# Kernel optimization log

Measured on AMD Instinct MI355X. Metric: run time of the kernel, lower is better.

## Reference

```python
import jax, jax.numpy as jnp
import numpy as np

SCALES = (3, 5, 7)

def _avg_pool3d_same(x, k):
    # stride-1 avg_pool3d with padding k//2, count_include_pad=True (torch default).
    # For odd k <= dim this preserves the spatial size, so the subsequent
    # F.interpolate to the input size is an exact identity.
    p = k // 2
    s = jax.lax.reduce_window(
        x, 0.0, jax.lax.add,
        window_dimensions=(1, 1, k, k, k),
        window_strides=(1, 1, 1, 1, 1),
        padding=[(0, 0), (0, 0), (p, p), (p, p), (p, p)])
    return s * (1.0 / float(k ** 3))

def setup_inputs() -> dict:
    key = jax.random.key(0)
    k1, k2 = jax.random.split(key)
    B, C, D, H, W = 2, 48, 64, 64, 64
    x = jax.random.normal(k1, (B, C, D, H, W), dtype=jnp.float32)
    fuse_w = jax.random.normal(k2, (1, len(SCALES) * C), dtype=jnp.float32) * 0.05
    fuse_b = jnp.zeros((1,), dtype=jnp.float32)
    return {"x": x, "fuse_w": fuse_w, "fuse_b": fuse_b}

def reference(x, fuse_w, fuse_b):
    # Multi-scale stride-1 average pooling (sizes preserved -> interp is identity)
    pooled = [_avg_pool3d_same(x, k) for k in SCALES]   # each (B, C, D, H, W)
    cat = jnp.concatenate(pooled, axis=1)               # (B, 3C, D, H, W)
    # 1x1x1 conv to a single channel, then sigmoid
    out = jnp.einsum('bcdhw,oc->bodhw', cat, fuse_w) + fuse_b[None, :, None, None, None]
    return jax.nn.sigmoid(out)                          # (B, 1, D, H, W)
```

## Files before the change

### kernel.cpp

```cpp
#include <hip/hip_runtime.h>
#include <math.h>

#define CH       48
#define DIM      64
#define SPATIAL  (DIM * DIM * DIM)
#define NB       2
#define VOL      (NB * SPATIAL)
#define NS       3
#define ROWS     16
#define ZT_PLANE 4096
#define DT       8
#define DTH      (DT + 6)

typedef float f4 __attribute__((ext_vector_type(4)));

__global__ __launch_bounds__(256) void kA(
        const float* __restrict__ x,
        const float* __restrict__ fw,
        float* __restrict__ zt) {
    __shared__ float sw[NS * CH];
    __shared__ f4 tile[NS][ROWS][16];
    const int tid = threadIdx.x;
    if (tid < NS * CH) sw[tid] = fw[tid];
    __syncthreads();

    const int lr  = tid >> 4;
    const int lw  = tid & 15;
    const int row = blockIdx.x * ROWS + lr;
    const int b   = row >> 12;
    const int dh  = row & 4095;

    const f4* xp = (const f4*)x
        + (size_t)b * CH * (SPATIAL / 4)
        + (size_t)dh * 16 + lw;

    f4 a0 = {0,0,0,0}, a1 = {0,0,0,0}, a2 = {0,0,0,0};
    #pragma unroll 16
    for (int c = 0; c < CH; ++c) {
        f4 v = xp[(size_t)c * (SPATIAL / 4)];
        a0 += sw[c] * v;
        a1 += sw[CH + c] * v;
        a2 += sw[2 * CH + c] * v;
    }
    tile[0][lr][lw] = a0;
    tile[1][lr][lw] = a1;
    tile[2][lr][lw] = a2;
    __syncthreads();

    f4* zt4 = (f4*)zt;
    const f4 zero = {0,0,0,0};
    #pragma unroll
    for (int s = 0; s < NS; ++s) {
        f4 m1 = (lw > 0)  ? tile[s][lr][lw - 1] : zero;
        f4 m0 = tile[s][lr][lw];
        f4 p1 = (lw < 15) ? tile[s][lr][lw + 1] : zero;
        float f[12] = {m1.x, m1.y, m1.z, m1.w,
                       m0.x, m0.y, m0.z, m0.w,
                       p1.x, p1.y, p1.z, p1.w};
        const int p = s + 1;
        f4 r;
        #pragma unroll
        for (int j = 0; j < 4; ++j) {
            float acc = 0.f;
            #pragma unroll
            for (int i = -3; i <= 3; ++i)
                if (i >= -p && i <= p) acc += f[4 + j + i];
            r[j] = acc;
        }
        zt4[((size_t)(s * NB + b) * 16 + lw) * ZT_PLANE + dh] = r;
    }
}

__global__ __launch_bounds__(256) void kB(
        const float* __restrict__ zt,
        const float* __restrict__ fb,
        float* __restrict__ out) {
    __shared__ f4 tile[NS][DTH][DIM];
    const int tid = threadIdx.x;
    const int bid = blockIdx.x;
    const int w4  = bid & 15;
    const int d0  = ((bid >> 4) & 7) * DT;
    const int b   = bid >> 7;

    const f4* zt4 = (const f4*)zt;
    #pragma unroll
    for (int s = 0; s < NS; ++s) {
        const f4* src = zt4 + ((size_t)(s * NB + b) * 16 + w4) * ZT_PLANE;
        #pragma unroll
        for (int t = 0; t < (DTH * DIM + 255) / 256; ++t) {
            int i = tid + t * 256;
            if (i < DTH * DIM) {
                int dd = i >> 6, h = i & 63;
                int gd = d0 - 3 + dd;
                f4 v = {0,0,0,0};
                if (gd >= 0 && gd < DIM) v = src[gd * 64 + h];
                tile[s][dd][h] = v;
            }
        }
    }
    __syncthreads();

    const int NITEM = NS * DTH * DIM;
    f4 acc[11];
    #pragma unroll
    for (int t = 0; t < 11; ++t) {
        int j = tid + t * 256;
        f4 a = {0,0,0,0};
        if (j < NITEM) {
            int s   = j / (DTH * DIM);
            int rem = j - s * (DTH * DIM);
            int dd  = rem >> 6, h = rem & 63;
            int p   = s + 1;
            int lo  = h - p; if (lo < 0)  lo = 0;
            int hi  = h + p; if (hi > 63) hi = 63;
            for (int hh = lo; hh <= hi; ++hh) a += tile[s][dd][hh];
        }
        acc[t] = a;
    }
    __syncthreads();
    #pragma unroll
    for (int t = 0; t < 11; ++t) {
        int j = tid + t * 256;
        if (j < NITEM) {
            int s   = j / (DTH * DIM);
            int rem = j - s * (DTH * DIM);
            tile[s][rem >> 6][rem & 63] = acc[t];
        }
    }
    __syncthreads();

    const float inv[NS] = {1.f / 27.f, 1.f / 125.f, 1.f / 343.f};
    const float bias = fb[0];
    f4* out4 = (f4*)out;
    #pragma unroll
    for (int t = 0; t < DT * DIM / 256; ++t) {
        int j   = tid + t * 256;
        int ddp = j >> 6, h = j & 63;
        int d   = d0 + ddp;
        f4 a2 = {bias, bias, bias, bias};
        #pragma unroll
        for (int s = 0; s < NS; ++s) {
            int p = s + 1;
            f4 a = {0,0,0,0};
            for (int i = -3; i <= 3; ++i)
                if (i >= -p && i <= p) a += tile[s][ddp + 3 + i][h];
            a2 += a * inv[s];
        }
        f4 r;
        #pragma unroll
        for (int jj = 0; jj < 4; ++jj) r[jj] = 1.f / (1.f + __expf(-a2[jj]));
        __builtin_nontemporal_store(r,
            &out4[(size_t)b * (SPATIAL / 4) + (size_t)d * 1024 + h * 16 + w4]);
    }
}

extern "C" void kernel_launch(void* const* d_in, const int* in_sizes, int n_in,
                              void* d_out, int out_size, void* d_ws, size_t ws_size,
                              hipStream_t stream) {
    const float* x  = (const float*)d_in[0];
    const float* fw = (const float*)d_in[1];
    const float* fb = (const float*)d_in[2];
    float* out = (float*)d_out;

    float* zt = (float*)d_ws;

    kA<<<(NB * DIM * DIM * DIM / ROWS) / 64, 256, 0, stream>>>(x, fw, zt);
    kB<<<NB * 16 * (DIM / DT), 256, 0, stream>>>(zt, fb, out);
}
```

Baseline: 33.27 us.

## Split channel reduction across thread groups and shrink tiles for more blocks

kA now has each block cover 4 rows instead of 16, and the 48-channel reduction is split across 4 channel groups of 64 threads. The partial sums are combined through shared memory, and the x loads become nontemporal. kB halves the depth tile, so there are twice as many blocks and each thread writes one output. The aim is more blocks and shorter per-thread dependency chains to hide memory latency. The cost is an extra shared-memory reduction with a sync, and a larger depth halo overhead in kB.

New measurement: 33.24 us. About the same (-0.1%).

```diff
diff --git a/kernel.cpp b/kernel.cpp
--- a/kernel.cpp
+++ b/kernel.cpp
@@ -7,10 +7,16 @@
 #define NB       2
 #define VOL      (NB * SPATIAL)
 #define NS       3
-#define ROWS     16
+#define CSLAB    (SPATIAL / 4)
+
+#define ROWS     4
+#define CG       4
+#define CPG      (CH / CG)
+
 #define ZT_PLANE 4096
-#define DT       8
+#define DT       4
 #define DTH      (DT + 6)
+#define NITEM    (NS * DTH * DIM)
 
 typedef float f4 __attribute__((ext_vector_type(4)));
 
@@ -19,41 +25,48 @@
         const float* __restrict__ fw,
         float* __restrict__ zt) {
     __shared__ float sw[NS * CH];
-    __shared__ f4 tile[NS][ROWS][16];
+    __shared__ f4 part[CG][NS][ROWS][16];
+    __shared__ f4 red[NS][ROWS][16];
     const int tid = threadIdx.x;
     if (tid < NS * CH) sw[tid] = fw[tid];
     __syncthreads();
 
-    const int lr  = tid >> 4;
-    const int lw  = tid & 15;
-    const int row = blockIdx.x * ROWS + lr;
-    const int b   = row >> 12;
-    const int dh  = row & 4095;
+    const int lw   = tid & 15;
+    const int lr   = (tid >> 4) & 3;
+    const int cg   = tid >> 6;
+    const int row0 = blockIdx.x * ROWS;
+    const int b    = row0 >> 12;
+    const int dh   = (row0 & 4095) + lr;
 
     const f4* xp = (const f4*)x
-        + (size_t)b * CH * (SPATIAL / 4)
+        + (size_t)(b * CH + cg * CPG) * CSLAB
         + (size_t)dh * 16 + lw;
 
     f4 a0 = {0,0,0,0}, a1 = {0,0,0,0}, a2 = {0,0,0,0};
-    #pragma unroll 16
-    for (int c = 0; c < CH; ++c) {
-        f4 v = xp[(size_t)c * (SPATIAL / 4)];
-        a0 += sw[c] * v;
-        a1 += sw[CH + c] * v;
-        a2 += sw[2 * CH + c] * v;
+    #pragma unroll
+    for (int c = 0; c < CPG; ++c) {
+        f4 v = __builtin_nontemporal_load(&xp[(size_t)c * CSLAB]);
+        const int cc = cg * CPG + c;
+        a0 += sw[cc] * v;
+        a1 += sw[CH + cc] * v;
+        a2 += sw[2 * CH + cc] * v;
     }
-    tile[0][lr][lw] = a0;
-    tile[1][lr][lw] = a1;
-    tile[2][lr][lw] = a2;
+    part[cg][0][lr][lw] = a0;
+    part[cg][1][lr][lw] = a1;
+    part[cg][2][lr][lw] = a2;
     __syncthreads();
 
-    f4* zt4 = (f4*)zt;
-    const f4 zero = {0,0,0,0};
-    #pragma unroll
-    for (int s = 0; s < NS; ++s) {
-        f4 m1 = (lw > 0)  ? tile[s][lr][lw - 1] : zero;
-        f4 m0 = tile[s][lr][lw];
-        f4 p1 = (lw < 15) ? tile[s][lr][lw + 1] : zero;
+    const int s = tid >> 6;
+    if (tid < 192) {
+        red[s][lr][lw] = part[0][s][lr][lw] + part[1][s][lr][lw]
+                       + part[2][s][lr][lw] + part[3][s][lr][lw];
+    }
+    __syncthreads();
+    if (tid < 192) {
+        const f4 zero = {0,0,0,0};
+        f4 m1 = (lw > 0)  ? red[s][lr][lw - 1] : zero;
+        f4 m0 = red[s][lr][lw];
+        f4 p1 = (lw < 15) ? red[s][lr][lw + 1] : zero;
         float f[12] = {m1.x, m1.y, m1.z, m1.w,
                        m0.x, m0.y, m0.z, m0.w,
                        p1.x, p1.y, p1.z, p1.w};
@@ -67,7 +80,7 @@
                 if (i >= -p && i <= p) acc += f[4 + j + i];
             r[j] = acc;
         }
-        zt4[((size_t)(s * NB + b) * 16 + lw) * ZT_PLANE + dh] = r;
+        ((f4*)zt)[((size_t)(s * NB + b) * 16 + lw) * ZT_PLANE + dh] = r;
     }
 }
 
@@ -79,8 +92,8 @@
     const int tid = threadIdx.x;
     const int bid = blockIdx.x;
     const int w4  = bid & 15;
-    const int d0  = ((bid >> 4) & 7) * DT;
-    const int b   = bid >> 7;
+    const int d0  = ((bid >> 4) & 15) * DT;
+    const int b   = bid >> 8;
 
     const f4* zt4 = (const f4*)zt;
     #pragma unroll
@@ -100,10 +113,9 @@
     }
     __syncthreads();
 
-    const int NITEM = NS * DTH * DIM;
-    f4 acc[11];
+    f4 acc[(NITEM + 255) / 256];
     #pragma unroll
-    for (int t = 0; t < 11; ++t) {
+    for (int t = 0; t < (NITEM + 255) / 256; ++t) {
         int j = tid + t * 256;
         f4 a = {0,0,0,0};
         if (j < NITEM) {
@@ -119,7 +131,7 @@
     }
     __syncthreads();
     #pragma unroll
-    for (int t = 0; t < 11; ++t) {
+    for (int t = 0; t < (NITEM + 255) / 256; ++t) {
         int j = tid + t * 256;
         if (j < NITEM) {
             int s   = j / (DTH * DIM);
@@ -131,27 +143,23 @@
 
     const float inv[NS] = {1.f / 27.f, 1.f / 125.f, 1.f / 343.f};
     const float bias = fb[0];
-    f4* out4 = (f4*)out;
+    const int ddp = tid >> 6, h = tid & 63;
+    const int d   = d0 + ddp;
+    f4 a2 = {bias, bias, bias, bias};
     #pragma unroll
-    for (int t = 0; t < DT * DIM / 256; ++t) {
-        int j   = tid + t * 256;
-        int ddp = j >> 6, h = j & 63;
-        int d   = d0 + ddp;
-        f4 a2 = {bias, bias, bias, bias};
+    for (int s = 0; s < NS; ++s) {
+        int p = s + 1;
+        f4 a = {0,0,0,0};
         #pragma unroll
-        for (int s = 0; s < NS; ++s) {
-            int p = s + 1;
-            f4 a = {0,0,0,0};
-            for (int i = -3; i <= 3; ++i)
-                if (i >= -p && i <= p) a += tile[s][ddp + 3 + i][h];
-            a2 += a * inv[s];
-        }
-        f4 r;
-        #pragma unroll
-        for (int jj = 0; jj < 4; ++jj) r[jj] = 1.f / (1.f + __expf(-a2[jj]));
-        __builtin_nontemporal_store(r,
-            &out4[(size_t)b * (SPATIAL / 4) + (size_t)d * 1024 + h * 16 + w4]);
+        for (int i = -3; i <= 3; ++i)
+            if (i >= -p && i <= p) a += tile[s][ddp + 3 + i][h];
+        a2 += a * inv[s];
     }
+    f4 r;
+    #pragma unroll
+    for (int jj = 0; jj < 4; ++jj) r[jj] = 1.f / (1.f + __expf(-a2[jj]));
+    __builtin_nontemporal_store(r,
+        &((f4*)out)[(size_t)b * (SPATIAL / 4) + (size_t)d * 1024 + h * 16 + w4]);
 }
 
 extern "C" void kernel_launch(void* const* d_in, const int* in_sizes, int n_in,
@@ -164,6 +172,6 @@
 
     float* zt = (float*)d_ws;
 
-    kA<<<(NB * DIM * DIM * DIM / ROWS) / 64, 256, 0, stream>>>(x, fw, zt);
+    kA<<<NB * DIM * DIM * DIM / DIM / ROWS * DIM / DIM, 256, 0, stream>>>(x, fw, zt);
     kB<<<NB * 16 * (DIM / DT), 256, 0, stream>>>(zt, fb, out);
 }
```
